# Kernel tuning notes

Hardware: AMD Instinct MI355X
Metric: run time of the kernel (lower is better)

The kernel has to match this reference:

```python
import jax, jax.numpy as jnp
import numpy as np

B, T, C, H = 4, 2048, 1024, 16
D = C // H  # head dim = 64


def setup_inputs() -> dict:
    key = jax.random.key(0)
    ks = jax.random.split(key, 8)
    s = 1.0 / np.sqrt(C)
    return {
        "x": jax.random.normal(ks[0], (B, T, C), jnp.float32),
        "mask": jax.random.randint(ks[1], (B, T), 0, 2, jnp.int32),
        "Wq": jax.random.normal(ks[2], (C, C), jnp.float32) * s,
        "bq": jnp.zeros((C,), jnp.float32),
        "Wk": jax.random.normal(ks[3], (C, C), jnp.float32) * s,
        "bk": jnp.zeros((C,), jnp.float32),
        "Wv": jax.random.normal(ks[4], (C, C), jnp.float32) * s,
        "bv": jnp.zeros((C,), jnp.float32),
    }


def reference(x, mask, Wq, bq, Wk, bk, Wv, bv):
    # QKV projections (nn.Linear: x @ W.T + b); W stored here as [out,in] -> use W.T
    q = x @ Wq.T + bq
    k = x @ Wk.T + bk
    v = x @ Wv.T + bv
    # split heads: [B,T,C] -> [B,H,T,D]
    q = q.reshape(B, T, H, D).transpose(0, 2, 1, 3)
    k = k.reshape(B, T, H, D).transpose(0, 2, 1, 3)
    v = v.reshape(B, T, H, D).transpose(0, 2, 1, 3)
    # scaled dot-product attention scores [B,H,T,T]
    attn = jnp.einsum("bhqd,bhkd->bhqk", q, k) / jnp.sqrt(jnp.float32(D))
    # additive mask over key positions: attn - inf*(1-mask), expressed stably
    big_neg = jnp.float32(-1e30)
    attn = jnp.where(mask[:, None, None, :] > 0, attn, big_neg)
    attn = jax.nn.softmax(attn, axis=-1)
    # dropout p=0 -> identity
    y = jnp.einsum("bhqk,bhkd->bhqd", attn, v)
    # merge heads: [B,H,T,D] -> [B,T,C]
    return y.transpose(0, 2, 1, 3).reshape(B, T, C)
```

## Files before the change

kernel.cpp:

```cpp
#include <hip/hip_runtime.h>
#include <stdint.h>

#define BB 4
#define TT 2048
#define CC 1024
#define HH 16
#define DD 64
#define MM (BB * TT)

typedef unsigned short u16;
typedef unsigned int   u32;
typedef __attribute__((ext_vector_type(8))) short short8;
typedef _Float16 half8  __attribute__((ext_vector_type(8)));
typedef __fp16   fp16x2 __attribute__((ext_vector_type(2)));
typedef __attribute__((ext_vector_type(4))) float f32x4;
typedef __attribute__((ext_vector_type(4))) unsigned short u16x4;
typedef __attribute__((ext_vector_type(4))) unsigned int u32x4;

#if __has_builtin(__builtin_amdgcn_exp2f)
#define EXP2(x) __builtin_amdgcn_exp2f(x)
#else
#define EXP2(x) __expf(0.69314718055994531f * (x))
#endif

__device__ inline u16 f2bf(float f) {
    union { float f; unsigned u; } v; v.f = f;
    unsigned r = 0x7fffu + ((v.u >> 16) & 1u);
    return (u16)((v.u + r) >> 16);
}
__device__ inline u16 f2h(float f) {
    union { _Float16 h; u16 u; } c; c.h = (_Float16)f; return c.u;
}
__device__ inline u32 pkh(float a, float b) {
    union { fp16x2 h; u32 u; } c;
    c.h = __builtin_amdgcn_cvt_pkrtz(a, b);
    return c.u;
}

#define NX (MM * CC / 4)
#define NW (CC * CC / 4)
__global__ void cvt_all(const float* __restrict__ x,  const float* __restrict__ Wq,
                        const float* __restrict__ Wk, const float* __restrict__ Wv,
                        u16* __restrict__ xb, u16* __restrict__ Wb) {
    int i = blockIdx.x * blockDim.x + threadIdx.x;
    const float* src; u16* dst; int j;
    if (i < NX)               { src = x;  dst = xb;                       j = i; }
    else if (i < NX + NW)     { src = Wq; dst = Wb;                       j = i - NX; }
    else if (i < NX + 2 * NW) { src = Wk; dst = Wb + (size_t)CC * CC;     j = i - NX - NW; }
    else if (i < NX + 3 * NW) { src = Wv; dst = Wb + (size_t)2 * CC * CC; j = i - NX - 2 * NW; }
    else return;
    float4 v = ((const float4*)src)[j];
    u16x4 o;
    o.x = f2bf(v.x); o.y = f2bf(v.y); o.z = f2bf(v.z); o.w = f2bf(v.w);
    ((u16x4*)dst)[j] = o;
}

__global__ void qkv_gemm(const u16* __restrict__ xb, const u16* __restrict__ Wb,
                         const float* __restrict__ bq, const float* __restrict__ bk,
                         const float* __restrict__ bv,
                         u16* __restrict__ Qh, u16* __restrict__ Kh, u16* __restrict__ Vt)
{
    const int z = blockIdx.z;
    const u16* W = Wb + (size_t)z * CC * CC;
    const float* bias = (z == 0) ? bq : ((z == 1) ? bk : bv);
    const float scale = (z == 0) ? 0.18033688011112042f : 1.0f;

    __shared__ __align__(16) u16 As[128][32];
    __shared__ __align__(16) u16 Bs[128][32];

    const int tid = threadIdx.x;
    const int l  = tid & 63, w = tid >> 6;
    const int wm = w >> 1,  wn = w & 1;
    const int lr = l & 15,  lq = l >> 4;
    const int m0 = blockIdx.y * 128, n0 = blockIdx.x * 128;

    f32x4 acc[4][4] = {};

    const u16* aLDS = (z == 2) ? &As[0][0] : &Bs[0][0];
    const u16* bLDS = (z == 2) ? &Bs[0][0] : &As[0][0];

    for (int kt = 0; kt < CC; kt += 32) {
        __syncthreads();
        #pragma unroll
        for (int r = 0; r < 2; ++r) {
            int c   = (r * 4 + w) * 64 + l;
            int row = c >> 2, kc = c & 3;
            const u16* ga = xb + (size_t)(m0 + row) * CC + kt + kc * 8;
            __builtin_amdgcn_global_load_lds(
                (const __attribute__((address_space(1))) void*)ga,
                (__attribute__((address_space(3))) void*)(&As[0][0] + (size_t)c * 8), 16, 0, 0);
            const u16* gb = W + (size_t)(n0 + row) * CC + kt + kc * 8;
            __builtin_amdgcn_global_load_lds(
                (const __attribute__((address_space(1))) void*)gb,
                (__attribute__((address_space(3))) void*)(&Bs[0][0] + (size_t)c * 8), 16, 0, 0);
        }
        __syncthreads();

        short8 af[4], bfr[4];
        #pragma unroll
        for (int mi = 0; mi < 4; ++mi)
            af[mi] = *(const short8*)(aLDS + (size_t)(wm * 64 + mi * 16 + lr) * 32 + lq * 8);
        #pragma unroll
        for (int ni = 0; ni < 4; ++ni)
            bfr[ni] = *(const short8*)(bLDS + (size_t)(wn * 64 + ni * 16 + lr) * 32 + lq * 8);
        #pragma unroll
        for (int mi = 0; mi < 4; ++mi)
            #pragma unroll
            for (int ni = 0; ni < 4; ++ni)
                acc[mi][ni] = __builtin_amdgcn_mfma_f32_16x16x32_bf16(
                    af[mi], bfr[ni], acc[mi][ni], 0, 0, 0);
    }

    if (z == 2) {
        #pragma unroll
        for (int ni = 0; ni < 4; ++ni) {
            int n = n0 + wn * 64 + ni * 16 + lr;
            float bvv = bias[n];
            int h = n >> 6, d = n & 63;
            #pragma unroll
            for (int mi = 0; mi < 4; ++mi) {
                int mbase = m0 + wm * 64 + mi * 16 + lq * 4;
                int b = mbase >> 11, t0 = mbase & (TT - 1);
                u16x4 pkv;
                #pragma unroll
                for (int r = 0; r < 4; ++r)
                    pkv[r] = f2h(acc[mi][ni][r] + bvv);
                *(u16x4*)&Vt[((size_t)(b * HH + h) * DD + d) * TT + t0] = pkv;
            }
        }
    } else {
        u16* out = (z == 0) ? Qh : Kh;
        #pragma unroll
        for (int mi = 0; mi < 4; ++mi) {
            int nb = n0 + wm * 64 + mi * 16 + lq * 4;
            float4 b4 = *(const float4*)&bias[nb];
            int h = nb >> 6, d0 = nb & 63;
            #pragma unroll
            for (int ni = 0; ni < 4; ++ni) {
                int m = m0 + wn * 64 + ni * 16 + lr;
                int b = m >> 11, t = m & (TT - 1);
                u16x4 pkv;
                pkv.x = f2h((acc[mi][ni][0] + b4.x) * scale);
                pkv.y = f2h((acc[mi][ni][1] + b4.y) * scale);
                pkv.z = f2h((acc[mi][ni][2] + b4.z) * scale);
                pkv.w = f2h((acc[mi][ni][3] + b4.w) * scale);
                *(u16x4*)&out[((size_t)(b * HH + h) * TT + t) * DD + d0] = pkv;
            }
        }
    }
}

__global__ __launch_bounds__(256, 2)
void attn_kernel(const u16* __restrict__ Qh, const u16* __restrict__ Kh,
                 const u16* __restrict__ Vt, const int* __restrict__ mask,
                 float* __restrict__ out)
{
    const int qt = blockIdx.x;
    const int h  = blockIdx.y;
    const int b  = blockIdx.z;
    const int tid = threadIdx.x;
    const int l  = tid & 63, w = tid >> 6;
    const int lr = l & 15,  lq = l >> 4;

    __shared__ __align__(16) u16 Ks[2][32][72];
    __shared__ __align__(16) u16 Vs[2][80][40];

    const size_t base = (size_t)(b * HH + h) * TT * DD;
    const int q0 = qt * 256 + w * 64;

    half8 qf[4][2];
    #pragma unroll
    for (int qg = 0; qg < 4; ++qg)
        #pragma unroll
        for (int c = 0; c < 2; ++c)
            qf[qg][c] = *(const half8*)(Qh + base + (size_t)(q0 + qg * 16 + lr) * DD
                                        + c * 32 + lq * 8);

    const int kk = tid >> 3, dc = tid & 7;
    u16* k_dst0 = &Ks[0][kk][dc * 8];
    const u16* k_base = Kh + base + (size_t)kk * DD + dc * 8;
    const int vd = tid >> 2, vck = tid & 3;
    const int s0c = ((2 * vck) & 3) * 8 + (vck >> 1) * 4;
    const int s1c = ((2 * vck + 1) & 3) * 8 + (vck >> 1) * 4;
    u16* v_dst0a = &Vs[0][vd][s0c];
    u16* v_dst0b = &Vs[0][vd][s1c];
    const u16* v_base = Vt + base + (size_t)vd * TT + vck * 8;
    const int* mbase_p = mask + b * TT + 4 * lq;

    for (int i = tid; i < 16 * 40; i += 256) {
        (&Vs[0][64][0])[i] = 0x3C00;
        (&Vs[1][64][0])[i] = 0x3C00;
    }

    {
        half8 k0 = *(const half8*)k_base;
        half8 v0 = *(const half8*)v_base;
        *(half8*)k_dst0 = k0;
        u16x4 va = { (u16)((u32x4&)v0)[0], (u16)(((u32x4&)v0)[0] >> 16),
                     (u16)((u32x4&)v0)[1], (u16)(((u32x4&)v0)[1] >> 16) };
        u16x4 vb = { (u16)((u32x4&)v0)[2], (u16)(((u32x4&)v0)[2] >> 16),
                     (u16)((u32x4&)v0)[3], (u16)(((u32x4&)v0)[3] >> 16) };
        *(u16x4*)v_dst0a = va;
        *(u16x4*)v_dst0b = vb;
    }

    f32x4 o[4][5] = {};

    const int NT = TT / 32;
    __syncthreads();

    for (int kt = 0; kt < NT; ++kt) {
        const int p = kt & 1;
        int ktn = (kt + 1 < NT) ? kt + 1 : NT - 1;
        half8 kreg = *(const half8*)(k_base + (size_t)ktn * 32 * DD);
        half8 vreg = *(const half8*)(v_base + ktn * 32);
        int4 ma = *(const int4*)(mbase_p + kt * 32);
        int4 mb = *(const int4*)(mbase_p + kt * 32 + 16);

        half8 kf[2][2];
        #pragma unroll
        for (int kg = 0; kg < 2; ++kg)
            #pragma unroll
            for (int c = 0; c < 2; ++c)
                kf[kg][c] = *(const half8*)&Ks[p][kg * 16 + lr][c * 32 + lq * 8];

        f32x4 s[2][4];
        #pragma unroll
        for (int kg = 0; kg < 2; ++kg)
            #pragma unroll
            for (int qg = 0; qg < 4; ++qg) {
                f32x4 zz = {};
                zz = __builtin_amdgcn_mfma_f32_16x16x32_f16(kf[kg][0], qf[qg][0], zz, 0, 0, 0);
                zz = __builtin_amdgcn_mfma_f32_16x16x32_f16(kf[kg][1], qf[qg][1], zz, 0, 0, 0);
                s[kg][qg] = zz;
            }

        const u32 am0 = ((u32)(-ma.x) & 0xFFFFu) | ((u32)(-ma.y) << 16);
        const u32 am1 = ((u32)(-ma.z) & 0xFFFFu) | ((u32)(-ma.w) << 16);
        const u32 am2 = ((u32)(-mb.x) & 0xFFFFu) | ((u32)(-mb.y) << 16);
        const u32 am3 = ((u32)(-mb.z) & 0xFFFFu) | ((u32)(-mb.w) << 16);

        half8 pf[4];
        #pragma unroll
        for (int qg = 0; qg < 4; ++qg) {
            u32x4 pk;
            pk[0] = pkh(EXP2(s[0][qg][0]), EXP2(s[0][qg][1])) & am0;
            pk[1] = pkh(EXP2(s[0][qg][2]), EXP2(s[0][qg][3])) & am1;
            pk[2] = pkh(EXP2(s[1][qg][0]), EXP2(s[1][qg][1])) & am2;
            pk[3] = pkh(EXP2(s[1][qg][2]), EXP2(s[1][qg][3])) & am3;
            pf[qg] = (half8&)pk;
        }

        #pragma unroll
        for (int dg = 0; dg < 5; ++dg) {
            half8 vf = *(const half8*)&Vs[p][dg * 16 + lr][lq * 8];
            #pragma unroll
            for (int qg = 0; qg < 4; ++qg)
                o[qg][dg] = __builtin_amdgcn_mfma_f32_16x16x32_f16(pf[qg], vf, o[qg][dg], 0, 0, 0);
        }

        *(half8*)(k_dst0 + (p ^ 1) * (32 * 72)) = kreg;
        u16x4 va = { (u16)((u32x4&)vreg)[0], (u16)(((u32x4&)vreg)[0] >> 16),
                     (u16)((u32x4&)vreg)[1], (u16)(((u32x4&)vreg)[1] >> 16) };
        u16x4 vb = { (u16)((u32x4&)vreg)[2], (u16)(((u32x4&)vreg)[2] >> 16),
                     (u16)((u32x4&)vreg)[3], (u16)(((u32x4&)vreg)[3] >> 16) };
        *(u16x4*)(v_dst0a + (p ^ 1) * (80 * 40)) = va;
        *(u16x4*)(v_dst0b + (p ^ 1) * (80 * 40)) = vb;
        __syncthreads();
    }

    #pragma unroll
    for (int qg = 0; qg < 4; ++qg)
        #pragma unroll
        for (int r = 0; r < 4; ++r) {
            float inv = 1.f / o[qg][4][r];
            int t = q0 + qg * 16 + lq * 4 + r;
            float* op = out + (size_t)(b * TT + t) * CC + h * DD;
            #pragma unroll
            for (int dg = 0; dg < 4; ++dg)
                op[dg * 16 + lr] = o[qg][dg][r] * inv;
        }
}

extern "C" void kernel_launch(void* const* d_in, const int* in_sizes, int n_in,
                              void* d_out, int out_size, void* d_ws, size_t ws_size,
                              hipStream_t stream) {
    const float* x    = (const float*)d_in[0];
    const int*   mask = (const int*)d_in[1];
    const float* Wq   = (const float*)d_in[2];
    const float* bq   = (const float*)d_in[3];
    const float* Wk   = (const float*)d_in[4];
    const float* bk   = (const float*)d_in[5];
    const float* Wv   = (const float*)d_in[6];
    const float* bv   = (const float*)d_in[7];
    float* out = (float*)d_out;

    u16* xb = (u16*)d_ws;
    u16* Wb = xb + (size_t)MM * CC;
    u16* Qh = Wb + (size_t)3 * CC * CC;
    u16* Kh = Qh + (size_t)MM * CC;
    u16* Vt = Kh + (size_t)MM * CC;

    {
        int total = NX + 3 * NW;
        cvt_all<<<(total + 255) / 256, 256, 0, stream>>>(x, Wq, Wk, Wv, xb, Wb);
    }

    qkv_gemm<<<dim3(CC / 128, MM / 128, 3), 256, 0, stream>>>(xb, Wb, bq, bk, bv, Qh, Kh, Vt);

    attn_kernel<<<dim3(TT / 256, HH, BB), 256, 0, stream>>>(Qh, Kh, Vt, mask, out);
}
```

Measured before the change: 249.9 us.

## Drop LDS staging in attention; load K/V fragments directly into registers

Each wave now loads its K and V MFMA fragments straight from global memory into registers, double-buffered across two tiles, instead of staging through shared memory with block-wide barriers. Per-wave query rows drop from 64 to 32, so the grid doubles and launch bounds rise to 3 blocks per SM. The row-sum column now comes from a constant ones vector rather than padded shared memory. The aim is to remove LDS traffic and __syncthreads stalls, at the cost of redundant global/L2 reads of K/V across waves and less MFMA work per load.

```diff
diff --git a/kernel.cpp b/kernel.cpp
--- a/kernel.cpp
+++ b/kernel.cpp
@@ -150,7 +150,69 @@
     }
 }
 
-__global__ __launch_bounds__(256, 2)
+struct KV {
+    half8 kf[2][2];
+    u16x4 va[4], vb[4];
+    int4  ma, mb;
+};
+
+__device__ __forceinline__ void load_tile(KV& F, const u16* k_base, const u16* v_base,
+                                          const int* mp, int t) {
+    const u16* kp = k_base + (size_t)t * (32 * DD);
+    #pragma unroll
+    for (int kg = 0; kg < 2; ++kg)
+        #pragma unroll
+        for (int c = 0; c < 2; ++c)
+            F.kf[kg][c] = *(const half8*)(kp + kg * 16 * DD + c * 32);
+    const u16* vp = v_base + t * 32;
+    #pragma unroll
+    for (int dg = 0; dg < 4; ++dg) {
+        F.va[dg] = *(const u16x4*)(vp + (size_t)dg * 16 * TT);
+        F.vb[dg] = *(const u16x4*)(vp + (size_t)dg * 16 * TT + 16);
+    }
+    F.ma = *(const int4*)(mp + t * 32);
+    F.mb = *(const int4*)(mp + t * 32 + 16);
+}
+
+__device__ __forceinline__ void compute_tile(const KV& F, const half8 (&qf)[2][2],
+                                             const half8 ones, f32x4 (&o)[2][5]) {
+    f32x4 s[2][2];
+    #pragma unroll
+    for (int kg = 0; kg < 2; ++kg)
+        #pragma unroll
+        for (int qg = 0; qg < 2; ++qg) {
+            f32x4 zz = {};
+            zz = __builtin_amdgcn_mfma_f32_16x16x32_f16(F.kf[kg][0], qf[qg][0], zz, 0, 0, 0);
+            zz = __builtin_amdgcn_mfma_f32_16x16x32_f16(F.kf[kg][1], qf[qg][1], zz, 0, 0, 0);
+            s[kg][qg] = zz;
+        }
+    const u32 am0 = ((u32)(-F.ma.x) & 0xFFFFu) | ((u32)(-F.ma.y) << 16);
+    const u32 am1 = ((u32)(-F.ma.z) & 0xFFFFu) | ((u32)(-F.ma.w) << 16);
+    const u32 am2 = ((u32)(-F.mb.x) & 0xFFFFu) | ((u32)(-F.mb.y) << 16);
+    const u32 am3 = ((u32)(-F.mb.z) & 0xFFFFu) | ((u32)(-F.mb.w) << 16);
+    half8 pf[2];
+    #pragma unroll
+    for (int qg = 0; qg < 2; ++qg) {
+        u32x4 pk;
+        pk[0] = pkh(EXP2(s[0][qg][0]), EXP2(s[0][qg][1])) & am0;
+        pk[1] = pkh(EXP2(s[0][qg][2]), EXP2(s[0][qg][3])) & am1;
+        pk[2] = pkh(EXP2(s[1][qg][0]), EXP2(s[1][qg][1])) & am2;
+        pk[3] = pkh(EXP2(s[1][qg][2]), EXP2(s[1][qg][3])) & am3;
+        pf[qg] = (half8&)pk;
+    }
+    #pragma unroll
+    for (int qg = 0; qg < 2; ++qg) {
+        #pragma unroll
+        for (int dg = 0; dg < 4; ++dg) {
+            union { half8 h; u16x4 q[2]; } vu;
+            vu.q[0] = F.va[dg]; vu.q[1] = F.vb[dg];
+            o[qg][dg] = __builtin_amdgcn_mfma_f32_16x16x32_f16(pf[qg], vu.h, o[qg][dg], 0, 0, 0);
+        }
+        o[qg][4] = __builtin_amdgcn_mfma_f32_16x16x32_f16(pf[qg], ones, o[qg][4], 0, 0, 0);
+    }
+}
+
+__global__ __launch_bounds__(256, 3)
 void attn_kernel(const u16* __restrict__ Qh, const u16* __restrict__ Kh,
                  const u16* __restrict__ Vt, const int* __restrict__ mask,
                  float* __restrict__ out)
@@ -162,115 +224,39 @@
     const int l  = tid & 63, w = tid >> 6;
     const int lr = l & 15,  lq = l >> 4;
 
-    __shared__ __align__(16) u16 Ks[2][32][72];
-    __shared__ __align__(16) u16 Vs[2][80][40];
-
     const size_t base = (size_t)(b * HH + h) * TT * DD;
-    const int q0 = qt * 256 + w * 64;
-
-    half8 qf[4][2];
-    #pragma unroll
-    for (int qg = 0; qg < 4; ++qg)
+    const int q0 = qt * 128 + w * 32;
+
+    half8 qf[2][2];
+    #pragma unroll
+    for (int qg = 0; qg < 2; ++qg)
         #pragma unroll
         for (int c = 0; c < 2; ++c)
             qf[qg][c] = *(const half8*)(Qh + base + (size_t)(q0 + qg * 16 + lr) * DD
                                         + c * 32 + lq * 8);
 
-    const int kk = tid >> 3, dc = tid & 7;
-    u16* k_dst0 = &Ks[0][kk][dc * 8];
-    const u16* k_base = Kh + base + (size_t)kk * DD + dc * 8;
-    const int vd = tid >> 2, vck = tid & 3;
-    const int s0c = ((2 * vck) & 3) * 8 + (vck >> 1) * 4;
-    const int s1c = ((2 * vck + 1) & 3) * 8 + (vck >> 1) * 4;
-    u16* v_dst0a = &Vs[0][vd][s0c];
-    u16* v_dst0b = &Vs[0][vd][s1c];
-    const u16* v_base = Vt + base + (size_t)vd * TT + vck * 8;
-    const int* mbase_p = mask + b * TT + 4 * lq;
-
-    for (int i = tid; i < 16 * 40; i += 256) {
-        (&Vs[0][64][0])[i] = 0x3C00;
-        (&Vs[1][64][0])[i] = 0x3C00;
-    }
-
-    {
-        half8 k0 = *(const half8*)k_base;
-        half8 v0 = *(const half8*)v_base;
-        *(half8*)k_dst0 = k0;
-        u16x4 va = { (u16)((u32x4&)v0)[0], (u16)(((u32x4&)v0)[0] >> 16),
-                     (u16)((u32x4&)v0)[1], (u16)(((u32x4&)v0)[1] >> 16) };
-        u16x4 vb = { (u16)((u32x4&)v0)[2], (u16)(((u32x4&)v0)[2] >> 16),
-                     (u16)((u32x4&)v0)[3], (u16)(((u32x4&)v0)[3] >> 16) };
-        *(u16x4*)v_dst0a = va;
-        *(u16x4*)v_dst0b = vb;
-    }
-
-    f32x4 o[4][5] = {};
+    const u16* k_base = Kh + base + (size_t)lr * DD + lq * 8;
+    const u16* v_base = Vt + base + (size_t)lr * TT + 4 * lq;
+    const int* mp     = mask + b * TT + 4 * lq;
+
+    union { u32 u[4]; half8 h; } one_u;
+    one_u.u[0] = one_u.u[1] = one_u.u[2] = one_u.u[3] = 0x3C003C00u;
+    const half8 ones = one_u.h;
+
+    f32x4 o[2][5] = {};
 
     const int NT = TT / 32;
-    __syncthreads();
-
-    for (int kt = 0; kt < NT; ++kt) {
-        const int p = kt & 1;
-        int ktn = (kt + 1 < NT) ? kt + 1 : NT - 1;
-        half8 kreg = *(const half8*)(k_base + (size_t)ktn * 32 * DD);
-        half8 vreg = *(const half8*)(v_base + ktn * 32);
-        int4 ma = *(const int4*)(mbase_p + kt * 32);
-        int4 mb = *(const int4*)(mbase_p + kt * 32 + 16);
-
-        half8 kf[2][2];
-        #pragma unroll
-        for (int kg = 0; kg < 2; ++kg)
-            #pragma unroll
-            for (int c = 0; c < 2; ++c)
-                kf[kg][c] = *(const half8*)&Ks[p][kg * 16 + lr][c * 32 + lq * 8];
-
-        f32x4 s[2][4];
-        #pragma unroll
-        for (int kg = 0; kg < 2; ++kg)
-            #pragma unroll
-            for (int qg = 0; qg < 4; ++qg) {
-                f32x4 zz = {};
-                zz = __builtin_amdgcn_mfma_f32_16x16x32_f16(kf[kg][0], qf[qg][0], zz, 0, 0, 0);
-                zz = __builtin_amdgcn_mfma_f32_16x16x32_f16(kf[kg][1], qf[qg][1], zz, 0, 0, 0);
-                s[kg][qg] = zz;
-            }
-
-        const u32 am0 = ((u32)(-ma.x) & 0xFFFFu) | ((u32)(-ma.y) << 16);
-        const u32 am1 = ((u32)(-ma.z) & 0xFFFFu) | ((u32)(-ma.w) << 16);
-        const u32 am2 = ((u32)(-mb.x) & 0xFFFFu) | ((u32)(-mb.y) << 16);
-        const u32 am3 = ((u32)(-mb.z) & 0xFFFFu) | ((u32)(-mb.w) << 16);
-
-        half8 pf[4];
-        #pragma unroll
-        for (int qg = 0; qg < 4; ++qg) {
-            u32x4 pk;
-            pk[0] = pkh(EXP2(s[0][qg][0]), EXP2(s[0][qg][1])) & am0;
-            pk[1] = pkh(EXP2(s[0][qg][2]), EXP2(s[0][qg][3])) & am1;
-            pk[2] = pkh(EXP2(s[1][qg][0]), EXP2(s[1][qg][1])) & am2;
-            pk[3] = pkh(EXP2(s[1][qg][2]), EXP2(s[1][qg][3])) & am3;
-            pf[qg] = (half8&)pk;
-        }
-
-        #pragma unroll
-        for (int dg = 0; dg < 5; ++dg) {
-            half8 vf = *(const half8*)&Vs[p][dg * 16 + lr][lq * 8];
-            #pragma unroll
-            for (int qg = 0; qg < 4; ++qg)
-                o[qg][dg] = __builtin_amdgcn_mfma_f32_16x16x32_f16(pf[qg], vf, o[qg][dg], 0, 0, 0);
-        }
-
-        *(half8*)(k_dst0 + (p ^ 1) * (32 * 72)) = kreg;
-        u16x4 va = { (u16)((u32x4&)vreg)[0], (u16)(((u32x4&)vreg)[0] >> 16),
-                     (u16)((u32x4&)vreg)[1], (u16)(((u32x4&)vreg)[1] >> 16) };
-        u16x4 vb = { (u16)((u32x4&)vreg)[2], (u16)(((u32x4&)vreg)[2] >> 16),
-                     (u16)((u32x4&)vreg)[3], (u16)(((u32x4&)vreg)[3] >> 16) };
-        *(u16x4*)(v_dst0a + (p ^ 1) * (80 * 40)) = va;
-        *(u16x4*)(v_dst0b + (p ^ 1) * (80 * 40)) = vb;
-        __syncthreads();
-    }
-
-    #pragma unroll
-    for (int qg = 0; qg < 4; ++qg)
+    KV A, B;
+    load_tile(A, k_base, v_base, mp, 0);
+    for (int t = 0; t < NT; t += 2) {
+        load_tile(B, k_base, v_base, mp, t + 1);
+        compute_tile(A, qf, ones, o);
+        load_tile(A, k_base, v_base, mp, (t + 2 < NT) ? t + 2 : NT - 1);
+        compute_tile(B, qf, ones, o);
+    }
+
+    #pragma unroll
+    for (int qg = 0; qg < 2; ++qg)
         #pragma unroll
         for (int r = 0; r < 4; ++r) {
             float inv = 1.f / o[qg][4][r];
@@ -308,5 +294,5 @@
 
     qkv_gemm<<<dim3(CC / 128, MM / 128, 3), 256, 0, stream>>>(xb, Wb, bq, bk, bv, Qh, Kh, Vt);
 
-    attn_kernel<<<dim3(TT / 256, HH, BB), 256, 0, stream>>>(Qh, Kh, Vt, mask, out);
-}
+    attn_kernel<<<dim3(TT / 128, HH, BB), 256, 0, stream>>>(Qh, Kh, Vt, mask, out);
+}
```

Result: slower. 528.2 us (+111.3%).
